# Optimization experiments

Hardware: AMD Instinct MI355X
Metric: run time of the kernel (lower is better)

Reference implementation:

```python
import jax, jax.numpy as jnp
import numpy as np

P = 2          # SamplesLoss p=2
BLUR = 0.05    # eps_final = BLUR**P = 0.0025
SCALING = 0.8  # annealing factor per iteration (on the blur scale)


def _cost(x, y):
    # geomloss cost for p=2: |x - y|^2 / 2, shape (N, M)
    x2 = jnp.sum(x * x, axis=-1)
    y2 = jnp.sum(y * y, axis=-1)
    return 0.5 * (x2[:, None] + y2[None, :] - 2.0 * (x @ y.T))


def _softmin(eps, C, h):
    # -eps * log sum_j exp(h_j - C_ij / eps); h already contains log-weights
    return -eps * jax.nn.logsumexp(h[None, :] - C / eps, axis=1)


def _eps_schedule(x, y):
    # geomloss scaling_parameters / epsilon_schedule with diameter from bounding box
    xn, yn = np.asarray(x), np.asarray(y)
    mins = np.minimum(xn.min(0), yn.min(0))
    maxs = np.maximum(xn.max(0), yn.max(0))
    diameter = float(np.linalg.norm(maxs - mins))
    eps_list = ([diameter ** P]
                + [float(np.exp(e)) for e in np.arange(P * np.log(diameter), P * np.log(BLUR), P * np.log(SCALING))]
                + [BLUR ** P])
    return eps_list


def _sinkhorn_divergence(x, y, eps_list):
    # Debiased Sinkhorn divergence S_eps(x, y), geomloss sinkhorn_tensorized
    N, M = x.shape[0], y.shape[0]
    sg = jax.lax.stop_gradient
    C_xy, C_yx = _cost(x, y), _cost(y, x)
    C_xx, C_yy = _cost(x, sg(x)), _cost(y, sg(y))  # geomloss detaches 2nd arg
    # The annealing loop runs with autograd disabled in geomloss:
    Cxy_, Cyx_, Cxx_, Cyy_ = sg(C_xy), sg(C_yx), sg(C_xx), sg(C_yy)
    a_log = jnp.full((N,), -np.log(N), dtype=x.dtype)  # log uniform weights
    b_log = jnp.full((M,), -np.log(M), dtype=y.dtype)
    e0 = eps_list[0]
    f_aa = _softmin(e0, Cxx_, a_log)
    g_bb = _softmin(e0, Cyy_, b_log)
    g_ab = _softmin(e0, Cyx_, a_log)
    f_ba = _softmin(e0, Cxy_, b_log)
    for eps in eps_list:  # fixed schedule, not a data-dim loop
        ft_ba = _softmin(eps, Cxy_, b_log + g_ab / eps)
        gt_ab = _softmin(eps, Cyx_, a_log + f_ba / eps)
        ft_aa = _softmin(eps, Cxx_, a_log + f_aa / eps)
        gt_bb = _softmin(eps, Cyy_, b_log + g_bb / eps)
        f_ba, g_ab = 0.5 * (f_ba + ft_ba), 0.5 * (g_ab + gt_ab)
        f_aa, g_bb = 0.5 * (f_aa + ft_aa), 0.5 * (g_bb + gt_bb)
    # Final extrapolation step (the only one geomloss differentiates through):
    eps = eps_list[-1]
    f_ba, g_ab = (_softmin(eps, C_xy, sg(b_log + g_ab / eps)),
                  _softmin(eps, C_yx, sg(a_log + f_ba / eps)))
    f_aa = _softmin(eps, C_xx, sg(a_log + f_aa / eps))
    g_bb = _softmin(eps, C_yy, sg(b_log + g_bb / eps))
    # scal with uniform weights == mean
    return jnp.mean(f_ba - f_aa) + jnp.mean(g_ab - g_bb)


def setup_inputs() -> dict:
    key = jax.random.key(0)
    kx, kt = jax.random.split(key)
    x = jax.random.normal(kx, (4096, 64), dtype=jnp.float32)
    target = jax.random.normal(kt, (4096, 64), dtype=jnp.float32)
    return {"x": x, "target": target}


def reference(x, target):
    eps_list = _eps_schedule(x, target)  # concrete schedule from data diameter
    return _sinkhorn_divergence(x, target, eps_list)
```

## Files before the change

### kernel.cpp

```cpp
#include <hip/hip_runtime.h>
#include <math.h>

#define NPTS 4096
#define DIM  64
#define MAX_ITERS 37

#define ALOG (-8.317766166719343f)
#define L2E  (1.4426950408889634f)
#define LN2  (0.6931471805599453f)

#if __has_builtin(__builtin_amdgcn_exp2f)
#define EXP2F(x) __builtin_amdgcn_exp2f(x)
#else
#define EXP2F(x) exp2f(x)
#endif
#if __has_builtin(__builtin_amdgcn_logf)
#define LOG2F(x) __builtin_amdgcn_logf(x)
#else
#define LOG2F(x) log2f(x)
#endif

typedef _Float16 f16x8 __attribute__((ext_vector_type(8)));
typedef float    f32x4 __attribute__((ext_vector_type(4)));

__device__ __forceinline__ void multi_barrier(int* st, int idx, int nsub,
                                              int* lsense) {
    __syncthreads();
    if (threadIdx.x == 0) {
        int s = *lsense ^ 1;
        __threadfence();
        int sub = idx >> 5;
        int prev = __hip_atomic_fetch_add(st + sub * 16, 1, __ATOMIC_ACQ_REL,
                                          __HIP_MEMORY_SCOPE_AGENT);
        if (prev == 31) {
            int pm = __hip_atomic_fetch_add(st + 512, 1, __ATOMIC_ACQ_REL,
                                            __HIP_MEMORY_SCOPE_AGENT);
            if (pm == nsub - 1) {
                for (int i = 0; i < nsub; i++)
                    __hip_atomic_store(st + i * 16, 0, __ATOMIC_RELAXED,
                                       __HIP_MEMORY_SCOPE_AGENT);
                __hip_atomic_store(st + 512, 0, __ATOMIC_RELAXED,
                                   __HIP_MEMORY_SCOPE_AGENT);
                __hip_atomic_store(st + 544, s, __ATOMIC_RELEASE,
                                   __HIP_MEMORY_SCOPE_AGENT);
            } else {
                while (__hip_atomic_load(st + 544, __ATOMIC_ACQUIRE,
                                         __HIP_MEMORY_SCOPE_AGENT) != s)
                    __builtin_amdgcn_s_sleep(8);
            }
        } else {
            while (__hip_atomic_load(st + 544, __ATOMIC_ACQUIRE,
                                     __HIP_MEMORY_SCOPE_AGENT) != s)
                __builtin_amdgcn_s_sleep(8);
        }
        *lsense = s;
        __threadfence();
    }
    __syncthreads();
}

template <int TPB>
__global__ __launch_bounds__(256, (TPB == 1 ? 4 : 2)) void mega_kernel(
        const float* __restrict__ x, const float* __restrict__ y,
        _Float16* __restrict__ X16, _Float16* __restrict__ Y16,
        float* __restrict__ x2, float* __restrict__ y2,
        float* __restrict__ pmn, float* __restrict__ pmx,
        int* hdr, float* __restrict__ sched,
        float* __restrict__ F, float* __restrict__ H, float* __restrict__ P,
        int* bar, float* __restrict__ out)
{
    const int b  = blockIdx.x;
    const int tt = threadIdx.x;
    int senseG = 0, senseL = 0;

    int* stG;  int nsubG;
    int* stL;  int idxL; int nsubL;
    if (TPB == 1) {
        stG = bar + 2048; nsubG = 32;
        stL = bar + (b >> 9) * 1024; idxL = b & 511; nsubL = 16;
    } else {
        stG = bar + 2048; nsubG = 16;
        stL = stG; idxL = b; nsubL = 16;
    }
    int* senseLp = (TPB == 1) ? &senseL : &senseG;

    __shared__ float hs[512];
    __shared__ _Float16 Bs[2][64][72];

    for (int g = b * 256 + tt; g < NPTS * DIM; g += gridDim.x * 256) {
        float xv = x[g], yv = y[g];
        X16[g] = (_Float16)xv;
        Y16[g] = (_Float16)yv;
        float sx = xv * xv, sy = yv * yv;
        for (int o = 32; o > 0; o >>= 1) {
            sx += __shfl_xor(sx, o, 64);
            sy += __shfl_xor(sy, o, 64);
        }
        if ((tt & 63) == 0) { x2[g >> 6] = sx; y2[g >> 6] = sy; }
    }
    if (b < 128) {
        float mn = INFINITY, mx = -INFINITY;
        for (int gg = b * 256 + tt; gg < NPTS * DIM; gg += 128 * 256) {
            float v = x[gg]; mn = fminf(mn, v); mx = fmaxf(mx, v);
            float w = y[gg]; mn = fminf(mn, w); mx = fmaxf(mx, w);
        }
        float* smn = hs;
        float* smx = (float*)&Bs[0][0][0];
        smn[tt] = mn; smx[tt] = mx;
        __syncthreads();
        if (tt < 64) {
            for (int qq = 1; qq < 4; qq++) {
                mn = fminf(mn, smn[tt + 64 * qq]);
                mx = fmaxf(mx, smx[tt + 64 * qq]);
            }
            pmn[b * 64 + tt] = mn;
            pmx[b * 64 + tt] = mx;
        }
    }
    multi_barrier(stG, b, nsubG, &senseG);

    if (b == 0) {
        float* r2 = hs;
        if (tt < 64) {
            float mn = INFINITY, mx = -INFINITY;
            for (int bb = 0; bb < 128; bb++) {
                mn = fminf(mn, pmn[bb * 64 + tt]);
                mx = fmaxf(mx, pmx[bb * 64 + tt]);
            }
            float range = mx - mn;
            r2[tt] = range * range;
        }
        __syncthreads();
        if (tt == 0) {
            float ss = 0.f;
            for (int k = 0; k < 64; k++) ss += r2[k];
            float diam_f = sqrtf(ss);
            double diam = (double)diam_f;
            double start = 2.0 * log(diam);
            double stop  = 2.0 * log(0.05);
            double step  = 2.0 * log(0.8);
            int n_ar = (int)ceil((stop - start) / step);
            if (n_ar < 0) n_ar = 0;
            int ne = n_ar + 2;
            if (ne > 63) ne = 63;
            sched[0] = (float)(diam * diam);
            for (int k = 0; k < n_ar && (1 + k) < 63; k++)
                sched[1 + k] = (float)exp(start + step * (double)k);
            sched[ne - 1] = 0.0025f;
            for (int k = ne; k < 64; k++) sched[k] = 0.0025f;
            hdr[0] = ne;
        }
    }
    multi_barrier(stG, b, nsubG, &senseG);

    const int n_eps = *(volatile int*)hdr;

    const int wv = tt >> 6, lane = tt & 63, q = lane >> 4, lo = lane & 15;
    const int srow = tt >> 2, scol = (tt & 3) * 16;

    f16x8 a[TPB][2][2];
#pragma unroll
    for (int sub = 0; sub < TPB; sub++) {
        const int bt = b + 512 * sub;
        const int mat_ = bt >> 8, rb_ = (bt >> 3) & 31;
        const _Float16* Am = (mat_ == 0 || mat_ == 2) ? X16 : Y16;
        const int r0_ = rb_ * 128;
#pragma unroll
        for (int rt = 0; rt < 2; rt++) {
            const _Float16* ar = Am + (size_t)(r0_ + wv * 32 + rt * 16 + lo) * DIM + q * 8;
            a[sub][rt][0] = *(const f16x8*)ar;
            a[sub][rt][1] = *(const f16x8*)(ar + 32);
        }
    }

    for (int p = 0; p <= n_eps + 2; p++) {
        const int t = (p == 0) ? -2 : (p == n_eps + 2) ? -1 : (p - 1);
        const bool do_main = (t < 0) || (t < n_eps);

#pragma unroll
        for (int sub = 0; sub < TPB; sub++) {
            const int bt = b + 512 * sub;
            const int mat = bt >> 8, rb = (bt >> 3) & 31, cs = bt & 7;
            const _Float16* Bm = (mat == 1 || mat == 2) ? X16 : Y16;
            const int matc = (mat < 2) ? (1 - mat) : mat;
            const float* sqc = (matc == 0 || matc == 2) ? x2 : y2;
            const int c0 = cs * 512, r0 = rb * 128;
            const _Float16* Bsrc0 = Bm + (size_t)(c0 + srow) * DIM + scol;

            f16x8 t0a, t0b;
            if (do_main) {
                t0a = *(const f16x8*)Bsrc0;
                t0b = *(const f16x8*)(Bsrc0 + 8);
            }

            if (t == -2) {
                float inv2i = L2E / sched[0];
                for (int r = tt; r < 512; r += 256)
                    hs[r] = ALOG * L2E - 0.5f * sqc[c0 + r] * inv2i;
            } else if (t == -1) {
                for (int r = tt; r < 512; r += 256)
                    hs[r] = H[mat * 4096 + c0 + r];
            } else {
                int pp = (t == 0) ? 1 : ((t - 1) & 1);
                const float* Pm = P + pp * 262144;
                const float* Ps = Pm + 131072;
                float epsp = sched[(t == 0) ? 0 : (t - 1)];
                float inv2c = L2E / sched[t];
                for (int r = tt; r < 512; r += 256) {
                    int row = c0 + r;
                    int base = (matc * 8) * NPTS + row;
                    float M = -INFINITY;
#pragma unroll
                    for (int qq = 0; qq < 8; qq++) M = fmaxf(M, Pm[base + qq * NPTS]);
                    float S = 0.f;
#pragma unroll
                    for (int qq = 0; qq < 8; qq++)
                        S += Ps[base + qq * NPTS] * EXP2F(Pm[base + qq * NPTS] - M);
                    float sq = sqc[row];
                    float res = 0.5f * sq - epsp * LN2 * (M + LOG2F(S));
                    float fnew = (t == 0) ? res
                               : 0.5f * (F[((t - 1) & 1) * 16384 + matc * 4096 + row] + res);
                    float h = ALOG * L2E + (fnew - 0.5f * sq) * inv2c;
                    hs[r] = h;
                    if (rb == 0) {
                        F[(t & 1) * 16384 + matc * 4096 + row] = fnew;
                        H[mat * 4096 + row] = h;
                    }
                }
            }

            if (do_main) {
                int idx = (t == -2) ? 0 : ((t == -1) ? n_eps - 1 : t);
                float inv2 = L2E / sched[idx];

                *(f16x8*)&Bs[0][srow][scol]     = t0a;
                *(f16x8*)&Bs[0][srow][scol + 8] = t0b;

                float m[2][4], s[2][4];
#pragma unroll
                for (int rt = 0; rt < 2; rt++)
#pragma unroll
                    for (int r = 0; r < 4; r++) { m[rt][r] = -INFINITY; s[rt][r] = 0.f; }

                for (int ct = 0; ct < 8; ct++) {
                    __syncthreads();
                    f16x8 n0, n1;
                    if (ct < 7) {
                        const _Float16* src = Bsrc0 + (size_t)(ct + 1) * 64 * DIM;
                        n0 = *(const f16x8*)src;
                        n1 = *(const f16x8*)(src + 8);
                    }
                    const _Float16 (*Bt)[72] = Bs[ct & 1];
                    float v[2][4][4];
#pragma unroll
                    for (int cc = 0; cc < 4; cc++) {
                        const _Float16* br = &Bt[cc * 16 + lo][q * 8];
                        f16x8 b0 = *(const f16x8*)br;
                        f16x8 b1 = *(const f16x8*)(br + 32);
                        float hval = hs[ct * 64 + cc * 16 + lo];
#pragma unroll
                        for (int rt = 0; rt < 2; rt++) {
                            f32x4 acc = {0.f, 0.f, 0.f, 0.f};
                            acc = __builtin_amdgcn_mfma_f32_16x16x32_f16(a[sub][rt][0], b0, acc, 0, 0, 0);
                            acc = __builtin_amdgcn_mfma_f32_16x16x32_f16(a[sub][rt][1], b1, acc, 0, 0, 0);
#pragma unroll
                            for (int r = 0; r < 4; r++) v[rt][r][cc] = fmaf(acc[r], inv2, hval);
                        }
                    }
#pragma unroll
                    for (int rt = 0; rt < 2; rt++)
#pragma unroll
                        for (int r = 0; r < 4; r++) {
                            float v0 = v[rt][r][0], v1 = v[rt][r][1];
                            float v2 = v[rt][r][2], v3 = v[rt][r][3];
                            float lm = fmaxf(fmaxf(v0, v1), fmaxf(v2, v3));
                            if (__any(lm > m[rt][r] + 40.0f)) {
                                float nm = fmaxf(m[rt][r], lm);
                                s[rt][r] *= EXP2F(m[rt][r] - nm);
                                m[rt][r] = nm;
                            }
                            if (lm > m[rt][r] - 26.0f) {
                                float mm = m[rt][r];
                                s[rt][r] += (EXP2F(v0 - mm) + EXP2F(v1 - mm))
                                          + (EXP2F(v2 - mm) + EXP2F(v3 - mm));
                            }
                        }
                    if (ct < 7) {
                        *(f16x8*)&Bs[(ct + 1) & 1][srow][scol]     = n0;
                        *(f16x8*)&Bs[(ct + 1) & 1][srow][scol + 8] = n1;
                    }
                }

                float ml[2][4];
#pragma unroll
                for (int rt = 0; rt < 2; rt++)
#pragma unroll
                    for (int r = 0; r < 4; r++) ml[rt][r] = m[rt][r];
#pragma unroll
                for (int off = 1; off < 16; off <<= 1)
#pragma unroll
                    for (int rt = 0; rt < 2; rt++)
#pragma unroll
                        for (int r = 0; r < 4; r++)
                            m[rt][r] = fmaxf(m[rt][r], __shfl_xor(m[rt][r], off, 64));
#pragma unroll
                for (int rt = 0; rt < 2; rt++)
#pragma unroll
                    for (int r = 0; r < 4; r++)
                        s[rt][r] *= EXP2F(ml[rt][r] - m[rt][r]);
#pragma unroll
                for (int off = 1; off < 16; off <<= 1)
#pragma unroll
                    for (int rt = 0; rt < 2; rt++)
#pragma unroll
                        for (int r = 0; r < 4; r++)
                            s[rt][r] += __shfl_xor(s[rt][r], off, 64);

                if (lo == 0) {
                    int pw = (t == -1) ? (n_eps & 1) : ((t == -2) ? 1 : (t & 1));
                    float* Pw = P + pw * 262144;
                    float* Sw = Pw + 131072;
#pragma unroll
                    for (int rt = 0; rt < 2; rt++)
#pragma unroll
                        for (int r = 0; r < 4; r++) {
                            int row = r0 + wv * 32 + rt * 16 + q * 4 + r;
                            Pw[(mat * 8 + cs) * NPTS + row] = m[rt][r];
                            Sw[(mat * 8 + cs) * NPTS + row] = s[rt][r];
                        }
                }
            }
            __syncthreads();
        }
        multi_barrier(stL, idxL, nsubL, senseLp);
    }

    multi_barrier(stG, b, nsubG, &senseG);

    if (b < 64) {
        const float* Pm = P + (n_eps & 1) * 262144;
        const float* Ps = Pm + 131072;
        int g = b * 256 + tt;
        int fmat = g >> 12, row = g & 4095;
        float eps = sched[n_eps - 1];
        const float* sqr = (fmat == 0 || fmat == 2) ? x2 : y2;
        int base = (fmat * 8) * NPTS + row;
        float M = -INFINITY;
#pragma unroll
        for (int qq = 0; qq < 8; qq++) M = fmaxf(M, Pm[base + qq * NPTS]);
        float S = 0.f;
#pragma unroll
        for (int qq = 0; qq < 8; qq++)
            S += Ps[base + qq * NPTS] * EXP2F(Pm[base + qq * NPTS] - M);
        float res = 0.5f * sqr[row] - eps * LN2 * (M + LOG2F(S));
        float val = ((fmat < 2) ? res : -res) * (1.0f / NPTS);
        float* sh = hs;
        sh[tt] = val;
        __syncthreads();
        for (int o = 128; o > 0; o >>= 1) {
            if (tt < o) sh[tt] += sh[tt + o];
            __syncthreads();
        }
        if (tt == 0) atomicAdd(out, sh[0]);
    }
}

__global__ void minmax_part_kernel(const float* __restrict__ x,
                                   const float* __restrict__ y,
                                   float* __restrict__ partmn,
                                   float* __restrict__ partmx) {
    int t = threadIdx.x;
    int bid = blockIdx.x;
    int g0 = bid * 256 + t;
    const int total = NPTS * DIM;
    float mn = INFINITY, mx = -INFINITY;
    for (int g = g0; g < total; g += 128 * 256) {
        float v = x[g]; mn = fminf(mn, v); mx = fmaxf(mx, v);
        float w = y[g]; mn = fminf(mn, w); mx = fmaxf(mx, w);
    }
    __shared__ float smn[256], smx[256];
    smn[t] = mn; smx[t] = mx;
    __syncthreads();
    if (t < 64) {
        for (int q = 1; q < 4; q++) {
            mn = fminf(mn, smn[t + 64 * q]);
            mx = fmaxf(mx, smx[t + 64 * q]);
        }
        partmn[bid * 64 + t] = mn;
        partmx[bid * 64 + t] = mx;
    }
}

__global__ void schedule_kernel(const float* __restrict__ partmn,
                                const float* __restrict__ partmx,
                                int* __restrict__ hdr,
                                float* __restrict__ sched) {
    int d = threadIdx.x;
    float mn = INFINITY, mx = -INFINITY;
    for (int b = 0; b < 128; b++) {
        mn = fminf(mn, partmn[b * 64 + d]);
        mx = fmaxf(mx, partmx[b * 64 + d]);
    }
    float range = mx - mn;
    __shared__ float r2[64];
    r2[d] = range * range;
    __syncthreads();
    if (d == 0) {
        float ss = 0.f;
        for (int k = 0; k < 64; k++) ss += r2[k];
        float diam_f = sqrtf(ss);
        double diam = (double)diam_f;
        double start = 2.0 * log(diam);
        double stop  = 2.0 * log(0.05);
        double step  = 2.0 * log(0.8);
        int n_eps = (int)ceil((stop - start) / step);
        if (n_eps < 0) n_eps = 0;
        n_eps += 2;
        if (n_eps > 63) n_eps = 63;
        sched[0] = (float)(diam * diam);
        for (int k = 0; k < n_eps - 2 && (1 + k) < 63; k++)
            sched[1 + k] = (float)exp(start + step * (double)k);
        sched[n_eps - 1] = 0.0025f;
        for (int k = n_eps; k < 64; k++) sched[k] = 0.0025f;
        hdr[0] = n_eps;
    }
}

__global__ void sqnorm_kernel(const float* __restrict__ X, float* __restrict__ out) {
    int wave = (blockIdx.x * blockDim.x + threadIdx.x) >> 6;
    int lane = threadIdx.x & 63;
    if (wave >= NPTS) return;
    float v = X[wave * DIM + lane];
    float s = v * v;
    for (int o = 32; o > 0; o >>= 1) s += __shfl_xor(s, o, 64);
    if (lane == 0) out[wave] = s;
}

__global__ void cast_kernel(const float* __restrict__ x, const float* __restrict__ y,
                            _Float16* __restrict__ X16, _Float16* __restrict__ Y16) {
    int g = blockIdx.x * 256 + threadIdx.x;
    X16[g] = (_Float16)x[g];
    Y16[g] = (_Float16)y[g];
}

__global__ __launch_bounds__(256, 4) void pass_kernel(
        const _Float16* __restrict__ X16, const _Float16* __restrict__ Y16,
        const float* __restrict__ x2, const float* __restrict__ y2,
        float* __restrict__ F, float* __restrict__ H, float* __restrict__ P,
        const int* __restrict__ hdr, const float* __restrict__ sched, int t) {
    const int n_eps = hdr[0];
    if (t >= 0 && t > n_eps) return;

    int b = blockIdx.x;
    int mat = b >> 8, rb = (b >> 3) & 31, cs = b & 7;
    const _Float16* Am = (mat == 0 || mat == 2) ? X16 : Y16;
    const _Float16* Bm = (mat == 1 || mat == 2) ? X16 : Y16;
    int matc = (mat < 2) ? (1 - mat) : mat;
    const float* sqc = (matc == 0 || matc == 2) ? x2 : y2;

    __shared__ float hs[512];
    __shared__ _Float16 Bs[2][64][72];

    int tt = threadIdx.x;
    int c0 = cs * 512, r0 = rb * 128;

    if (t == -2) {
        float inv2i = L2E / sched[0];
        for (int r = tt; r < 512; r += 256)
            hs[r] = ALOG * L2E - 0.5f * sqc[c0 + r] * inv2i;
    } else if (t == -1) {
        for (int r = tt; r < 512; r += 256)
            hs[r] = H[mat * 4096 + c0 + r];
    } else {
        int pp = (t == 0) ? 1 : ((t - 1) & 1);
        const float* Pm = P + pp * 262144;
        const float* Ps = Pm + 131072;
        float epsp = sched[(t == 0) ? 0 : (t - 1)];
        float inv2c = L2E / sched[t];
        for (int r = tt; r < 512; r += 256) {
            int row = c0 + r;
            int base = (matc * 8) * NPTS + row;
            float M = -INFINITY;
#pragma unroll
            for (int q = 0; q < 8; q++) M = fmaxf(M, Pm[base + q * NPTS]);
            float S = 0.f;
#pragma unroll
            for (int q = 0; q < 8; q++)
                S += Ps[base + q * NPTS] * EXP2F(Pm[base + q * NPTS] - M);
            float sq = sqc[row];
            float res = 0.5f * sq - epsp * LN2 * (M + LOG2F(S));
            float fnew = (t == 0) ? res
                       : 0.5f * (F[((t - 1) & 1) * 16384 + matc * 4096 + row] + res);
            float h = ALOG * L2E + (fnew - 0.5f * sq) * inv2c;
            hs[r] = h;
            if (rb == 0) {
                F[(t & 1) * 16384 + matc * 4096 + row] = fnew;
                H[mat * 4096 + row] = h;
            }
        }
    }
    __syncthreads();
    if (t >= 0 && t >= n_eps) return;

    int idx = (t == -2) ? 0 : ((t == -1) ? n_eps - 1 : t);
    float inv2 = L2E / sched[idx];

    int wv = tt >> 6, lane = tt & 63, q = lane >> 4, lo = lane & 15;

    f16x8 a[2][2];
#pragma unroll
    for (int rt = 0; rt < 2; rt++) {
        const _Float16* ar = Am + (size_t)(r0 + wv * 32 + rt * 16 + lo) * DIM + q * 8;
        a[rt][0] = *(const f16x8*)ar;
        a[rt][1] = *(const f16x8*)(ar + 32);
    }

    int srow = tt >> 2, scol = (tt & 3) * 16;
    {
        const _Float16* src = Bm + (size_t)(c0 + srow) * DIM + scol;
        *(f16x8*)&Bs[0][srow][scol]     = *(const f16x8*)src;
        *(f16x8*)&Bs[0][srow][scol + 8] = *(const f16x8*)(src + 8);
    }

    float m[2][4], s[2][4];
#pragma unroll
    for (int rt = 0; rt < 2; rt++)
#pragma unroll
        for (int r = 0; r < 4; r++) { m[rt][r] = -INFINITY; s[rt][r] = 0.f; }

    for (int ct = 0; ct < 8; ct++) {
        __syncthreads();
        f16x8 n0, n1;
        if (ct < 7) {
            const _Float16* src = Bm + (size_t)(c0 + (ct + 1) * 64 + srow) * DIM + scol;
            n0 = *(const f16x8*)src;
            n1 = *(const f16x8*)(src + 8);
        }
        const _Float16 (*Bt)[72] = Bs[ct & 1];
        float v[2][4][4];
#pragma unroll
        for (int cc = 0; cc < 4; cc++) {
            const _Float16* br = &Bt[cc * 16 + lo][q * 8];
            f16x8 b0 = *(const f16x8*)br;
            f16x8 b1 = *(const f16x8*)(br + 32);
            float hval = hs[ct * 64 + cc * 16 + lo];
#pragma unroll
            for (int rt = 0; rt < 2; rt++) {
                f32x4 acc = {0.f, 0.f, 0.f, 0.f};
                acc = __builtin_amdgcn_mfma_f32_16x16x32_f16(a[rt][0], b0, acc, 0, 0, 0);
                acc = __builtin_amdgcn_mfma_f32_16x16x32_f16(a[rt][1], b1, acc, 0, 0, 0);
#pragma unroll
                for (int r = 0; r < 4; r++) v[rt][r][cc] = fmaf(acc[r], inv2, hval);
            }
        }
#pragma unroll
        for (int rt = 0; rt < 2; rt++)
#pragma unroll
            for (int r = 0; r < 4; r++) {
                float lm = fmaxf(fmaxf(v[rt][r][0], v[rt][r][1]),
                                 fmaxf(v[rt][r][2], v[rt][r][3]));
                if (lm > m[rt][r] - 26.0f) {
                    float nm = fmaxf(m[rt][r], lm);
                    float acc = s[rt][r] * EXP2F(m[rt][r] - nm);
                    acc += EXP2F(v[rt][r][0] - nm) + EXP2F(v[rt][r][1] - nm)
                         + EXP2F(v[rt][r][2] - nm) + EXP2F(v[rt][r][3] - nm);
                    m[rt][r] = nm; s[rt][r] = acc;
                }
            }
        if (ct < 7) {
            *(f16x8*)&Bs[(ct + 1) & 1][srow][scol]     = n0;
            *(f16x8*)&Bs[(ct + 1) & 1][srow][scol + 8] = n1;
        }
    }

#pragma unroll
    for (int off = 1; off < 16; off <<= 1) {
#pragma unroll
        for (int rt = 0; rt < 2; rt++)
#pragma unroll
            for (int r = 0; r < 4; r++) {
                float om = __shfl_xor(m[rt][r], off, 64);
                float os = __shfl_xor(s[rt][r], off, 64);
                float nm = fmaxf(m[rt][r], om);
                s[rt][r] = s[rt][r] * EXP2F(m[rt][r] - nm) + os * EXP2F(om - nm);
                m[rt][r] = nm;
            }
    }
    if (lo == 0) {
        int pw = (t == -1) ? (n_eps & 1) : ((t == -2) ? 1 : (t & 1));
        float* Pm = P + pw * 262144;
        float* Ps = Pm + 131072;
#pragma unroll
        for (int rt = 0; rt < 2; rt++)
#pragma unroll
            for (int r = 0; r < 4; r++) {
                int row = r0 + wv * 32 + rt * 16 + q * 4 + r;
                Pm[(mat * 8 + cs) * NPTS + row] = m[rt][r];
                Ps[(mat * 8 + cs) * NPTS + row] = s[rt][r];
            }
    }
}

__global__ void finalize_kernel(const float* __restrict__ P,
                                const float* __restrict__ x2, const float* __restrict__ y2,
                                const int* __restrict__ hdr, const float* __restrict__ sched,
                                float* __restrict__ out) {
    int n_eps = hdr[0];
    const float* Pm = P + (n_eps & 1) * 262144;
    const float* Ps = Pm + 131072;
    int g = blockIdx.x * 256 + threadIdx.x;
    int mat = g >> 12, row = g & 4095;
    float eps = sched[n_eps - 1];
    const float* sqr = (mat == 0 || mat == 2) ? x2 : y2;
    int base = (mat * 8) * NPTS + row;
    float M = -INFINITY;
#pragma unroll
    for (int q = 0; q < 8; q++) M = fmaxf(M, Pm[base + q * NPTS]);
    float S = 0.f;
#pragma unroll
    for (int q = 0; q < 8; q++) S += Ps[base + q * NPTS] * EXP2F(Pm[base + q * NPTS] - M);
    float res = 0.5f * sqr[row] - eps * LN2 * (M + LOG2F(S));
    float val = ((mat == 0 || mat == 1) ? res : -res) * (1.0f / NPTS);
    __shared__ float sh[256];
    sh[threadIdx.x] = val;
    __syncthreads();
    for (int o = 128; o > 0; o >>= 1) {
        if (threadIdx.x < o) sh[threadIdx.x] += sh[threadIdx.x + o];
        __syncthreads();
    }
    if (threadIdx.x == 0) atomicAdd(out, sh[0]);
}

extern "C" void kernel_launch(void* const* d_in, const int* in_sizes, int n_in,
                              void* d_out, int out_size, void* d_ws, size_t ws_size,
                              hipStream_t stream) {
    const float* x = (const float*)d_in[0];
    const float* y = (const float*)d_in[1];
    float* out = (float*)d_out;
    float* w = (float*)d_ws;

    int*   hdr   = (int*)w;
    float* sched = w + 16;
    float* pmn   = w + 80;
    float* pmx   = w + 8272;
    float* x2    = w + 16464;
    float* y2    = w + 20560;
    float* F     = w + 24656;
    float* H     = w + 57424;
    float* P     = w + 73808;
    _Float16* X16 = (_Float16*)(w + 598096);
    _Float16* Y16 = (_Float16*)(w + 729168);
    int*   bar   = (int*)(w + 860240);

    hipMemsetAsync(out, 0, sizeof(float), stream);
    hipMemsetAsync(bar, 0, 3 * 1024 * sizeof(int), stream);

    int occ1 = 0, occ2 = 0;
    (void)hipOccupancyMaxActiveBlocksPerMultiprocessor(&occ1, mega_kernel<1>, 256, 0);
    (void)hipOccupancyMaxActiveBlocksPerMultiprocessor(&occ2, mega_kernel<2>, 256, 0);

    if (occ1 >= 4) {
        hipLaunchKernelGGL((mega_kernel<1>), dim3(1024), dim3(256), 0, stream,
                           x, y, X16, Y16, x2, y2, pmn, pmx, hdr, sched, F, H, P, bar, out);
    } else if (occ2 >= 2) {
        hipLaunchKernelGGL((mega_kernel<2>), dim3(512), dim3(256), 0, stream,
                           x, y, X16, Y16, x2, y2, pmn, pmx, hdr, sched, F, H, P, bar, out);
    } else {
        hipLaunchKernelGGL(minmax_part_kernel, dim3(128), dim3(256), 0, stream, x, y, pmn, pmx);
        hipLaunchKernelGGL(schedule_kernel, dim3(1), dim3(64), 0, stream, pmn, pmx, hdr, sched);
        hipLaunchKernelGGL(sqnorm_kernel, dim3(1024), dim3(256), 0, stream, x, x2);
        hipLaunchKernelGGL(sqnorm_kernel, dim3(1024), dim3(256), 0, stream, y, y2);
        hipLaunchKernelGGL(cast_kernel, dim3(1024), dim3(256), 0, stream, x, y, X16, Y16);
        hipLaunchKernelGGL(pass_kernel, dim3(1024), dim3(256), 0, stream,
                           X16, Y16, x2, y2, F, H, P, hdr, sched, -2);
        for (int t = 0; t < MAX_ITERS; t++)
            hipLaunchKernelGGL(pass_kernel, dim3(1024), dim3(256), 0, stream,
                               X16, Y16, x2, y2, F, H, P, hdr, sched, t);
        hipLaunchKernelGGL(pass_kernel, dim3(1024), dim3(256), 0, stream,
                           X16, Y16, x2, y2, F, H, P, hdr, sched, -1);
        hipLaunchKernelGGL(finalize_kernel, dim3(64), dim3(256), 0, stream,
                           P, x2, y2, hdr, sched, out);
    }
}
```

Before: 962.0 us.

## Add 2048-block persistent megakernel with split barriers and 8 blocks per CU

Adds a new persistent kernel launched with 2048 blocks of 256 threads at 8 blocks per CU. Each block owns a 128-row by 256-column tile of one of the four cost matrices and computes it on the fly with f16 MFMA and an online log-sum-exp. The per-iteration grid barrier is split into two independent 1024-block groups, since each pair of coupled matrices only depends on its own data, and a global barrier is kept only for setup and finalize. The aim is more parallelism, better latency hiding and cheaper barriers. The cost is higher register pressure under the 8-block launch bound, extra workspace, and a fallback to the old paths when occupancy or workspace is too small.

```diff
diff --git a/kernel.cpp b/kernel.cpp
--- a/kernel.cpp
+++ b/kernel.cpp
@@ -59,6 +59,306 @@
     __syncthreads();
 }
 
+__device__ __forceinline__ void multi_barrier_g(int* st, int idx, int nsub,
+                                                int* lsense) {
+    __syncthreads();
+    if (threadIdx.x == 0) {
+        int s = *lsense ^ 1;
+        __threadfence();
+        int sub = idx >> 5;
+        int prev = __hip_atomic_fetch_add(st + sub * 16, 1, __ATOMIC_ACQ_REL,
+                                          __HIP_MEMORY_SCOPE_AGENT);
+        if (prev == 31) {
+            int pm = __hip_atomic_fetch_add(st + 1536, 1, __ATOMIC_ACQ_REL,
+                                            __HIP_MEMORY_SCOPE_AGENT);
+            if (pm == nsub - 1) {
+                for (int i = 0; i < nsub; i++)
+                    __hip_atomic_store(st + i * 16, 0, __ATOMIC_RELAXED,
+                                       __HIP_MEMORY_SCOPE_AGENT);
+                __hip_atomic_store(st + 1536, 0, __ATOMIC_RELAXED,
+                                   __HIP_MEMORY_SCOPE_AGENT);
+                __hip_atomic_store(st + 1600, s, __ATOMIC_RELEASE,
+                                   __HIP_MEMORY_SCOPE_AGENT);
+            } else {
+                while (__hip_atomic_load(st + 1600, __ATOMIC_ACQUIRE,
+                                         __HIP_MEMORY_SCOPE_AGENT) != s)
+                    __builtin_amdgcn_s_sleep(8);
+            }
+        } else {
+            while (__hip_atomic_load(st + 1600, __ATOMIC_ACQUIRE,
+                                     __HIP_MEMORY_SCOPE_AGENT) != s)
+                __builtin_amdgcn_s_sleep(8);
+        }
+        *lsense = s;
+        __threadfence();
+    }
+    __syncthreads();
+}
+
+__global__ __launch_bounds__(256, 8) void mega8_kernel(
+        const float* __restrict__ x, const float* __restrict__ y,
+        _Float16* __restrict__ X16, _Float16* __restrict__ Y16,
+        float* __restrict__ x2, float* __restrict__ y2,
+        float* __restrict__ pmn, float* __restrict__ pmx,
+        int* hdr, float* __restrict__ sched,
+        float* __restrict__ F, float* __restrict__ H, float* __restrict__ P,
+        int* bar, float* __restrict__ out)
+{
+    const int b  = blockIdx.x;
+    const int tt = threadIdx.x;
+    int senseG = 0, senseL = 0;
+
+    int* stL = bar + (b >> 10) * 2048;
+    int* stG = bar + 2 * 2048;
+    const int idxL = b & 1023;
+
+    __shared__ float hs[256];
+    __shared__ _Float16 Bs[2][64][72];
+
+    {
+        int g = b * 256 + tt;
+        if (g < NPTS * DIM) {
+            float xv = x[g], yv = y[g];
+            X16[g] = (_Float16)xv;
+            Y16[g] = (_Float16)yv;
+            float sx = xv * xv, sy = yv * yv;
+            for (int o = 32; o > 0; o >>= 1) {
+                sx += __shfl_xor(sx, o, 64);
+                sy += __shfl_xor(sy, o, 64);
+            }
+            if ((tt & 63) == 0) { x2[g >> 6] = sx; y2[g >> 6] = sy; }
+        }
+        if (b < 128) {
+            float mn = INFINITY, mx = -INFINITY;
+            for (int gg = b * 256 + tt; gg < NPTS * DIM; gg += 128 * 256) {
+                float v = x[gg]; mn = fminf(mn, v); mx = fmaxf(mx, v);
+                float w = y[gg]; mn = fminf(mn, w); mx = fmaxf(mx, w);
+            }
+            float* smn = hs;
+            float* smx = (float*)&Bs[0][0][0];
+            smn[tt] = mn; smx[tt] = mx;
+            __syncthreads();
+            if (tt < 64) {
+                for (int qq = 1; qq < 4; qq++) {
+                    mn = fminf(mn, smn[tt + 64 * qq]);
+                    mx = fmaxf(mx, smx[tt + 64 * qq]);
+                }
+                pmn[b * 64 + tt] = mn;
+                pmx[b * 64 + tt] = mx;
+            }
+        }
+    }
+    multi_barrier_g(stG, b, 64, &senseG);
+
+    if (b == 0) {
+        float* r2 = hs;
+        if (tt < 64) {
+            float mn = INFINITY, mx = -INFINITY;
+            for (int bb = 0; bb < 128; bb++) {
+                mn = fminf(mn, pmn[bb * 64 + tt]);
+                mx = fmaxf(mx, pmx[bb * 64 + tt]);
+            }
+            float range = mx - mn;
+            r2[tt] = range * range;
+        }
+        __syncthreads();
+        if (tt == 0) {
+            float ss = 0.f;
+            for (int k = 0; k < 64; k++) ss += r2[k];
+            float diam_f = sqrtf(ss);
+            double diam = (double)diam_f;
+            double start = 2.0 * log(diam);
+            double stop  = 2.0 * log(0.05);
+            double step  = 2.0 * log(0.8);
+            int n_ar = (int)ceil((stop - start) / step);
+            if (n_ar < 0) n_ar = 0;
+            int ne = n_ar + 2;
+            if (ne > 63) ne = 63;
+            sched[0] = (float)(diam * diam);
+            for (int k = 0; k < n_ar && (1 + k) < 63; k++)
+                sched[1 + k] = (float)exp(start + step * (double)k);
+            sched[ne - 1] = 0.0025f;
+            for (int k = ne; k < 64; k++) sched[k] = 0.0025f;
+            hdr[0] = ne;
+        }
+    }
+    multi_barrier_g(stG, b, 64, &senseG);
+
+    const int n_eps = *(volatile int*)hdr;
+
+    const int mat = b >> 9, rb = (b >> 4) & 31, cs = b & 15;
+    const _Float16* Am = (mat == 0 || mat == 2) ? X16 : Y16;
+    const _Float16* Bm = (mat == 1 || mat == 2) ? X16 : Y16;
+    const int matc = (mat < 2) ? (1 - mat) : mat;
+    const float* sqc = (matc == 0 || matc == 2) ? x2 : y2;
+    const int c0 = cs * 256, r0 = rb * 128;
+    const int wv = tt >> 6, lane = tt & 63, q = lane >> 4, lo = lane & 15;
+    const int srow = tt >> 2, scol = (tt & 3) * 16;
+
+    f16x8 a[2][2];
+#pragma unroll
+    for (int rt = 0; rt < 2; rt++) {
+        const _Float16* ar = Am + (size_t)(r0 + wv * 32 + rt * 16 + lo) * DIM + q * 8;
+        a[rt][0] = *(const f16x8*)ar;
+        a[rt][1] = *(const f16x8*)(ar + 32);
+    }
+    const _Float16* Bsrc0 = Bm + (size_t)(c0 + srow) * DIM + scol;
+
+    for (int p = 0; p <= n_eps + 2; p++) {
+        const int t = (p == 0) ? -2 : (p == n_eps + 2) ? -1 : (p - 1);
+        const bool do_main = (t < 0) || (t < n_eps);
+
+        f16x8 t0a, t0b;
+        if (do_main) {
+            t0a = *(const f16x8*)Bsrc0;
+            t0b = *(const f16x8*)(Bsrc0 + 8);
+        }
+
+        if (t == -2) {
+            float inv2i = L2E / sched[0];
+            hs[tt] = ALOG * L2E - 0.5f * sqc[c0 + tt] * inv2i;
+        } else if (t == -1) {
+            hs[tt] = H[mat * 4096 + c0 + tt];
+        } else {
+            int pp = (t == 0) ? 1 : ((t - 1) & 1);
+            const float* Pm = P + pp * 524288;
+            const float* Ps = Pm + 262144;
+            float epsp = sched[(t == 0) ? 0 : (t - 1)];
+            float inv2c = L2E / sched[t];
+            int row = c0 + tt;
+            int base = (matc * 16) * NPTS + row;
+            float M = -INFINITY;
+#pragma unroll
+            for (int qq = 0; qq < 16; qq++) M = fmaxf(M, Pm[base + qq * NPTS]);
+            float S = 0.f;
+#pragma unroll
+            for (int qq = 0; qq < 16; qq++)
+                S += Ps[base + qq * NPTS] * EXP2F(Pm[base + qq * NPTS] - M);
+            float sq = sqc[row];
+            float res = 0.5f * sq - epsp * LN2 * (M + LOG2F(S));
+            float fnew = (t == 0) ? res
+                       : 0.5f * (F[((t - 1) & 1) * 16384 + matc * 4096 + row] + res);
+            float h = ALOG * L2E + (fnew - 0.5f * sq) * inv2c;
+            hs[tt] = h;
+            if (rb == 0) {
+                F[(t & 1) * 16384 + matc * 4096 + row] = fnew;
+                H[mat * 4096 + row] = h;
+            }
+        }
+
+        if (do_main) {
+            int idx = (t == -2) ? 0 : ((t == -1) ? n_eps - 1 : t);
+            float inv2 = L2E / sched[idx];
+
+            *(f16x8*)&Bs[0][srow][scol]     = t0a;
+            *(f16x8*)&Bs[0][srow][scol + 8] = t0b;
+
+            float m[2] = { -INFINITY, -INFINITY };
+            float s[2] = { 0.f, 0.f };
+
+            for (int ct = 0; ct < 4; ct++) {
+                __syncthreads();
+                f16x8 n0, n1;
+                if (ct < 3) {
+                    const _Float16* src = Bsrc0 + (size_t)(ct + 1) * 64 * DIM;
+                    n0 = *(const f16x8*)src;
+                    n1 = *(const f16x8*)(src + 8);
+                }
+                const _Float16 (*Bt)[72] = Bs[ct & 1];
+#pragma unroll
+                for (int cc = 0; cc < 4; cc++) {
+                    const _Float16* br = &Bt[cc * 16 + lo][q * 8];
+                    f16x8 b0 = *(const f16x8*)br;
+                    f16x8 b1 = *(const f16x8*)(br + 32);
+                    f32x4 hv = *(const f32x4*)&hs[ct * 64 + cc * 16 + q * 4];
+#pragma unroll
+                    for (int rt = 0; rt < 2; rt++) {
+                        f32x4 acc = {0.f, 0.f, 0.f, 0.f};
+                        acc = __builtin_amdgcn_mfma_f32_16x16x32_f16(b0, a[rt][0], acc, 0, 0, 0);
+                        acc = __builtin_amdgcn_mfma_f32_16x16x32_f16(b1, a[rt][1], acc, 0, 0, 0);
+                        float v0 = fmaf(acc[0], inv2, hv[0]);
+                        float v1 = fmaf(acc[1], inv2, hv[1]);
+                        float v2 = fmaf(acc[2], inv2, hv[2]);
+                        float v3 = fmaf(acc[3], inv2, hv[3]);
+                        float lm = fmaxf(fmaxf(v0, v1), fmaxf(v2, v3));
+                        if (__any(lm > m[rt] + 40.0f)) {
+                            float nm = fmaxf(m[rt], lm);
+                            s[rt] *= EXP2F(m[rt] - nm);
+                            m[rt] = nm;
+                        }
+                        if (lm > m[rt] - 26.0f) {
+                            float mm = m[rt];
+                            s[rt] += (EXP2F(v0 - mm) + EXP2F(v1 - mm))
+                                   + (EXP2F(v2 - mm) + EXP2F(v3 - mm));
+                        }
+                    }
+                }
+                if (ct < 3) {
+                    *(f16x8*)&Bs[(ct + 1) & 1][srow][scol]     = n0;
+                    *(f16x8*)&Bs[(ct + 1) & 1][srow][scol + 8] = n1;
+                }
+            }
+
+            float ml[2] = { m[0], m[1] };
+#pragma unroll
+            for (int off = 16; off < 64; off <<= 1)
+#pragma unroll
+                for (int rt = 0; rt < 2; rt++)
+                    m[rt] = fmaxf(m[rt], __shfl_xor(m[rt], off, 64));
+#pragma unroll
+            for (int rt = 0; rt < 2; rt++)
+                s[rt] *= EXP2F(ml[rt] - m[rt]);
+#pragma unroll
+            for (int off = 16; off < 64; off <<= 1)
+#pragma unroll
+                for (int rt = 0; rt < 2; rt++)
+                    s[rt] += __shfl_xor(s[rt], off, 64);
+
+            if (q == 0) {
+                int pw = (t == -1) ? (n_eps & 1) : ((t == -2) ? 1 : (t & 1));
+                float* Pw = P + pw * 524288;
+                float* Sw = Pw + 262144;
+#pragma unroll
+                for (int rt = 0; rt < 2; rt++) {
+                    int row = r0 + wv * 32 + rt * 16 + lo;
+                    Pw[(mat * 16 + cs) * NPTS + row] = m[rt];
+                    Sw[(mat * 16 + cs) * NPTS + row] = s[rt];
+                }
+            }
+        }
+        multi_barrier_g(stL, idxL, 32, &senseL);
+    }
+
+    multi_barrier_g(stG, b, 64, &senseG);
+
+    if (b < 64) {
+        const float* Pm = P + (n_eps & 1) * 524288;
+        const float* Ps = Pm + 262144;
+        int g = b * 256 + tt;
+        int fmat = g >> 12, row = g & 4095;
+        float eps = sched[n_eps - 1];
+        const float* sqr = (fmat == 0 || fmat == 2) ? x2 : y2;
+        int base = (fmat * 16) * NPTS + row;
+        float M = -INFINITY;
+#pragma unroll
+        for (int qq = 0; qq < 16; qq++) M = fmaxf(M, Pm[base + qq * NPTS]);
+        float S = 0.f;
+#pragma unroll
+        for (int qq = 0; qq < 16; qq++)
+            S += Ps[base + qq * NPTS] * EXP2F(Pm[base + qq * NPTS] - M);
+        float res = 0.5f * sqr[row] - eps * LN2 * (M + LOG2F(S));
+        float val = ((fmat < 2) ? res : -res) * (1.0f / NPTS);
+        float* sh = hs;
+        sh[tt] = val;
+        __syncthreads();
+        for (int o = 128; o > 0; o >>= 1) {
+            if (tt < o) sh[tt] += sh[tt + o];
+            __syncthreads();
+        }
+        if (tt == 0) atomicAdd(out, sh[0]);
+    }
+}
+
 template <int TPB>
 __global__ __launch_bounds__(256, (TPB == 1 ? 4 : 2)) void mega_kernel(
         const float* __restrict__ x, const float* __restrict__ y,
@@ -648,36 +948,51 @@
     float* F     = w + 24656;
     float* H     = w + 57424;
     float* P     = w + 73808;
-    _Float16* X16 = (_Float16*)(w + 598096);
-    _Float16* Y16 = (_Float16*)(w + 729168);
-    int*   bar   = (int*)(w + 860240);
+
+    _Float16* X16c = (_Float16*)(w + 598096);
+    _Float16* Y16c = (_Float16*)(w + 729168);
+    int*      barc = (int*)(w + 860240);
+
+    _Float16* X16e = (_Float16*)(w + 1122384);
+    _Float16* Y16e = (_Float16*)(w + 1253456);
+    int*      bare = (int*)(w + 1384528);
+    const size_t ws_need_e = (size_t)(1384528 + 6144 + 64) * 4;
 
     hipMemsetAsync(out, 0, sizeof(float), stream);
-    hipMemsetAsync(bar, 0, 3 * 1024 * sizeof(int), stream);
-
-    int occ1 = 0, occ2 = 0;
+
+    int occ8 = 0, occ1 = 0, occ2 = 0;
+    (void)hipOccupancyMaxActiveBlocksPerMultiprocessor(&occ8, mega8_kernel, 256, 0);
     (void)hipOccupancyMaxActiveBlocksPerMultiprocessor(&occ1, mega_kernel<1>, 256, 0);
     (void)hipOccupancyMaxActiveBlocksPerMultiprocessor(&occ2, mega_kernel<2>, 256, 0);
 
-    if (occ1 >= 4) {
+    if (occ8 >= 8 && ws_size >= ws_need_e) {
+        hipMemsetAsync(bare, 0, 3 * 2048 * sizeof(int), stream);
+        hipLaunchKernelGGL(mega8_kernel, dim3(2048), dim3(256), 0, stream,
+                           x, y, X16e, Y16e, x2, y2, pmn, pmx, hdr, sched,
+                           F, H, P, bare, out);
+    } else if (occ1 >= 4) {
+        hipMemsetAsync(barc, 0, 3 * 1024 * sizeof(int), stream);
         hipLaunchKernelGGL((mega_kernel<1>), dim3(1024), dim3(256), 0, stream,
-                           x, y, X16, Y16, x2, y2, pmn, pmx, hdr, sched, F, H, P, bar, out);
+                           x, y, X16c, Y16c, x2, y2, pmn, pmx, hdr, sched,
+                           F, H, P, barc, out);
     } else if (occ2 >= 2) {
+        hipMemsetAsync(barc, 0, 3 * 1024 * sizeof(int), stream);
         hipLaunchKernelGGL((mega_kernel<2>), dim3(512), dim3(256), 0, stream,
-                           x, y, X16, Y16, x2, y2, pmn, pmx, hdr, sched, F, H, P, bar, out);
+                           x, y, X16c, Y16c, x2, y2, pmn, pmx, hdr, sched,
+                           F, H, P, barc, out);
     } else {
         hipLaunchKernelGGL(minmax_part_kernel, dim3(128), dim3(256), 0, stream, x, y, pmn, pmx);
         hipLaunchKernelGGL(schedule_kernel, dim3(1), dim3(64), 0, stream, pmn, pmx, hdr, sched);
         hipLaunchKernelGGL(sqnorm_kernel, dim3(1024), dim3(256), 0, stream, x, x2);
         hipLaunchKernelGGL(sqnorm_kernel, dim3(1024), dim3(256), 0, stream, y, y2);
-        hipLaunchKernelGGL(cast_kernel, dim3(1024), dim3(256), 0, stream, x, y, X16, Y16);
+        hipLaunchKernelGGL(cast_kernel, dim3(1024), dim3(256), 0, stream, x, y, X16c, Y16c);
         hipLaunchKernelGGL(pass_kernel, dim3(1024), dim3(256), 0, stream,
-                           X16, Y16, x2, y2, F, H, P, hdr, sched, -2);
+                           X16c, Y16c, x2, y2, F, H, P, hdr, sched, -2);
         for (int t = 0; t < MAX_ITERS; t++)
             hipLaunchKernelGGL(pass_kernel, dim3(1024), dim3(256), 0, stream,
-                               X16, Y16, x2, y2, F, H, P, hdr, sched, t);
+                               X16c, Y16c, x2, y2, F, H, P, hdr, sched, t);
         hipLaunchKernelGGL(pass_kernel, dim3(1024), dim3(256), 0, stream,
-                           X16, Y16, x2, y2, F, H, P, hdr, sched, -1);
+                           X16c, Y16c, x2, y2, F, H, P, hdr, sched, -1);
         hipLaunchKernelGGL(finalize_kernel, dim3(64), dim3(256), 0, stream,
                            P, x2, y2, hdr, sched, out);
     }
```

Result: no change. 959.4 us (-0.3%).
